# Kernel tuning notes

Hardware: AMD Instinct MI355X
Metric: run time of the kernel (lower is better)

Reference implementation:

```python
import jax, jax.numpy as jnp
import numpy as np

B, S, E, H = 8, 2048, 1024, 64

def setup_inputs() -> dict:
    key = jax.random.key(0)
    k1, k2, k3, k4 = jax.random.split(key, 4)
    scale = 0.02
    return {
        "x": jax.random.normal(k1, (B, S, E), dtype=jnp.float32),
        "Wq": jax.random.normal(k2, (E, H), dtype=jnp.float32) * scale,
        "Wk": jax.random.normal(k3, (E, H), dtype=jnp.float32) * scale,
        "Wv": jax.random.normal(k4, (E, H), dtype=jnp.float32) * scale,
    }

def reference(x, Wq, Wk, Wv):
    # x: [B, S, E]; projections to [B, S, H]
    q = jnp.einsum("bse,eh->bsh", x, Wq)
    k = jnp.einsum("bse,eh->bsh", x, Wk)
    v = jnp.einsum("bse,eh->bsh", x, Wv)
    head_size = Wq.shape[1]
    # NOTE: original divides by head_size (not sqrt(head_size))
    scores = jnp.einsum("bqh,bkh->bqk", q, k) / head_size  # [B, S, S]
    seq = q.shape[1]
    causal = jnp.tril(jnp.ones((seq, seq), dtype=bool))
    scores = jnp.where(causal, scores, -jnp.inf)
    attn = jax.nn.softmax(scores, axis=-1)
    # dropout p=0.0 (eval) -> identity
    return jnp.einsum("bqk,bkh->bqh", attn, v)
```

## Files before the change

### kernel.cpp

```cpp
#include <hip/hip_runtime.h>


typedef __bf16 bf16;
typedef bf16 bf16x8 __attribute__((ext_vector_type(8)));
typedef bf16 bf16x4 __attribute__((ext_vector_type(4)));
typedef float v4f __attribute__((ext_vector_type(4)));

#define MFMA_BF16 __builtin_amdgcn_mfma_f32_16x16x32_bf16

constexpr int SEQ = 2048, EDIM = 1024, HDIM = 64;
constexpr float SCALE_L2E = 1.4426950408889634f / 64.0f;

__global__ __launch_bounds__(256) void prep_w_kernel(
    const float* __restrict__ Wq, const float* __restrict__ Wk,
    const float* __restrict__ Wv, bf16* __restrict__ Wt) {
  int mat = blockIdx.x >> 5, kseg = blockIdx.x & 31;
  const float* src = mat == 0 ? Wq : (mat == 1 ? Wk : Wv);
  int n = threadIdx.x & 63;
  int k0 = kseg * 32 + (threadIdx.x >> 6) * 8;
  bf16x8 v;
#pragma unroll
  for (int j = 0; j < 8; ++j)
    v[j] = (bf16)src[(k0 + j) * 64 + n];
  *reinterpret_cast<bf16x8*>(Wt + (size_t)(mat * 64 + n) * EDIM + k0) = v;
}

__global__ __launch_bounds__(256) void proj_kernel(
    const float* __restrict__ x, const bf16* __restrict__ Wt,
    bf16* __restrict__ qw, bf16* __restrict__ kw, bf16* __restrict__ vT) {
  const int t = threadIdx.x;
  const int w = t >> 6, lane = t & 63, quad = lane >> 4, l16 = lane & 15;
  const int mi = w & 1, nh = w >> 1;
  const int m0 = blockIdx.x * 32;
  const int row = m0 + 16 * mi + l16;

  const float* xr = x + (size_t)row * EDIM + 8 * quad;
  const bf16* wB = Wt + (size_t)(96 * nh + l16) * EDIM + 8 * quad;

  v4f acc[6] = {};
  float4 aA[2][4];
  bf16x8 bReg[2][12];

  auto loadA = [&](int kk, int slot) {
    const float* p = xr + kk * 64;
    aA[slot][0] = *reinterpret_cast<const float4*>(p);
    aA[slot][1] = *reinterpret_cast<const float4*>(p + 4);
    aA[slot][2] = *reinterpret_cast<const float4*>(p + 32);
    aA[slot][3] = *reinterpret_cast<const float4*>(p + 36);
  };
  auto loadB = [&](int kk, int slot) {
#pragma unroll
    for (int nt = 0; nt < 6; ++nt)
#pragma unroll
      for (int ks = 0; ks < 2; ++ks)
        bReg[slot][2 * nt + ks] = *reinterpret_cast<const bf16x8*>(
            wB + (size_t)(16 * nt) * EDIM + kk * 64 + 32 * ks);
  };

  loadA(0, 0);
  loadB(0, 0);
  loadA(1, 1);
  loadB(1, 1);

#pragma unroll 2
  for (int kk = 0; kk < 16; ++kk) {
    const int buf = kk & 1;
    bf16x8 af[2];
#pragma unroll
    for (int ks = 0; ks < 2; ++ks) {
      float4 lo = aA[buf][2 * ks], hi = aA[buf][2 * ks + 1];
      af[ks][0] = (bf16)lo.x; af[ks][1] = (bf16)lo.y;
      af[ks][2] = (bf16)lo.z; af[ks][3] = (bf16)lo.w;
      af[ks][4] = (bf16)hi.x; af[ks][5] = (bf16)hi.y;
      af[ks][6] = (bf16)hi.z; af[ks][7] = (bf16)hi.w;
    }
    if (kk + 2 < 16) loadA(kk + 2, buf);
#pragma unroll
    for (int nt = 0; nt < 6; ++nt)
#pragma unroll
      for (int ks = 0; ks < 2; ++ks)
        acc[nt] = MFMA_BF16(af[ks], bReg[buf][2 * nt + ks], acc[nt], 0, 0, 0);
    if (kk + 2 < 16) loadB(kk + 2, buf);
  }

  const int token0 = m0 + 16 * mi + 4 * quad;
#pragma unroll
  for (int nt = 0; nt < 6; ++nt) {
    const int tl = 6 * nh + nt;
    if (tl < 4) {
      const int n = 16 * tl + l16;
#pragma unroll
      for (int r = 0; r < 4; ++r)
        qw[(size_t)(token0 + r) * HDIM + n] = (bf16)acc[nt][r];
    } else if (tl < 8) {
      const int n = 16 * (tl - 4) + l16;
#pragma unroll
      for (int r = 0; r < 4; ++r)
        kw[(size_t)(token0 + r) * HDIM + n] = (bf16)acc[nt][r];
    } else {
      const int hrow = 16 * (tl - 8) + l16;
      const int b = token0 >> 11, s0 = token0 & 2047;
      bf16x4 pk = {(bf16)acc[nt][0], (bf16)acc[nt][1], (bf16)acc[nt][2],
                   (bf16)acc[nt][3]};
      *reinterpret_cast<bf16x4*>(vT + ((size_t)(b * 64 + hrow)) * SEQ + s0) =
          pk;
    }
  }
}

__global__ __launch_bounds__(256) void attn_kernel(
    const bf16* __restrict__ qw, const bf16* __restrict__ kw,
    const bf16* __restrict__ vT, float* __restrict__ out) {
  const int batch = blockIdx.x & 7;
  const int pi = blockIdx.x >> 3;
  const int w = threadIdx.x >> 6;
  const int lane = threadIdx.x & 63;
  const int quad = lane >> 4, l16 = lane & 15;

  __shared__ __align__(16) bf16 p_lds[4][2][32][68];
  __shared__ __align__(16) float o_lds[3][32][68];
  __shared__ float l_lds[3][32];

  const bf16* qB = qw + (size_t)batch * SEQ * HDIM;
  const bf16* kB = kw + (size_t)batch * SEQ * HDIM;
  const bf16* vB = vT + (size_t)batch * HDIM * SEQ;

  for (int sp = 0; sp < 2; ++sp) {
    const int j = sp ? (63 - pi) : pi;
    const int q0 = 32 * j;
    const int T64 = (j + 2) >> 1;
    const int nw = (T64 > w) ? (((T64 - 1 - w) >> 2) + 1) : 0;

    bf16x8 aq[2][2];
#pragma unroll
    for (int mi = 0; mi < 2; ++mi)
#pragma unroll
      for (int kf = 0; kf < 2; ++kf)
        aq[mi][kf] = *reinterpret_cast<const bf16x8*>(
            qB + (size_t)(q0 + 16 * mi + l16) * HDIM + 32 * kf + 8 * quad);

    v4f accO[2][4] = {};
    float l_part[2][4] = {{0.f, 0.f, 0.f, 0.f}, {0.f, 0.f, 0.f, 0.f}};
    bf16x8 kfr[4][2];

    auto loadK = [&](int jt) {
#pragma unroll
      for (int nt = 0; nt < 4; ++nt)
#pragma unroll
        for (int kf = 0; kf < 2; ++kf)
          kfr[nt][kf] = *reinterpret_cast<const bf16x8*>(
              kB + (size_t)(64 * jt + 16 * nt + l16) * HDIM + 32 * kf +
              8 * quad);
    };
    auto qk_exp_stage = [&](int jt, int slot) {
      v4f s[2][4] = {};
#pragma unroll
      for (int mi = 0; mi < 2; ++mi)
#pragma unroll
        for (int nt = 0; nt < 4; ++nt) {
          s[mi][nt] = MFMA_BF16(aq[mi][0], kfr[nt][0], s[mi][nt], 0, 0, 0);
          s[mi][nt] = MFMA_BF16(aq[mi][1], kfr[nt][1], s[mi][nt], 0, 0, 0);
        }
      const bool last = (jt == T64 - 1);
#pragma unroll
      for (int mi = 0; mi < 2; ++mi)
#pragma unroll
        for (int nt = 0; nt < 4; ++nt)
#pragma unroll
          for (int r = 0; r < 4; ++r) {
            float p = __builtin_amdgcn_exp2f(s[mi][nt][r] * SCALE_L2E);
            if (last &&
                (64 * jt + 16 * nt + l16 > q0 + 16 * mi + 4 * quad + r))
              p = 0.f;
            l_part[mi][r] += p;
            p_lds[w][slot][16 * mi + 4 * quad + r][16 * nt + l16] = (bf16)p;
          }
    };

    if (nw > 0) {
      loadK(w);
      qk_exp_stage(w, 0);
    }
    for (int i = 0; i < nw; ++i) {
      const int jt = w + 4 * i;
      const int k0 = 64 * jt;
      if (i + 1 < nw) loadK(jt + 4);
      bf16x8 vfr[4][2];
#pragma unroll
      for (int nt = 0; nt < 4; ++nt)
#pragma unroll
        for (int kc = 0; kc < 2; ++kc)
          vfr[nt][kc] = *reinterpret_cast<const bf16x8*>(
              vB + (size_t)(16 * nt + l16) * SEQ + k0 + 32 * kc + 8 * quad);
      asm volatile("s_waitcnt lgkmcnt(0)" ::: "memory");
      bf16x8 pa[2][2];
#pragma unroll
      for (int mi = 0; mi < 2; ++mi)
#pragma unroll
        for (int kc = 0; kc < 2; ++kc)
          pa[mi][kc] = *reinterpret_cast<const bf16x8*>(
              &p_lds[w][i & 1][16 * mi + l16][32 * kc + 8 * quad]);
      if (i + 1 < nw) qk_exp_stage(jt + 4, (i + 1) & 1);
#pragma unroll
      for (int mi = 0; mi < 2; ++mi)
#pragma unroll
        for (int nt = 0; nt < 4; ++nt) {
          accO[mi][nt] = MFMA_BF16(pa[mi][0], vfr[nt][0], accO[mi][nt], 0, 0, 0);
          accO[mi][nt] = MFMA_BF16(pa[mi][1], vfr[nt][1], accO[mi][nt], 0, 0, 0);
        }
    }

#pragma unroll
    for (int mi = 0; mi < 2; ++mi)
#pragma unroll
      for (int r = 0; r < 4; ++r) {
        float s = l_part[mi][r];
        s += __shfl_xor(s, 1, 16);
        s += __shfl_xor(s, 2, 16);
        s += __shfl_xor(s, 4, 16);
        s += __shfl_xor(s, 8, 16);
        l_part[mi][r] = s;
      }

    __syncthreads();
    if (w > 0) {
#pragma unroll
      for (int mi = 0; mi < 2; ++mi)
#pragma unroll
        for (int nt = 0; nt < 4; ++nt)
#pragma unroll
          for (int r = 0; r < 4; ++r)
            o_lds[w - 1][16 * mi + 4 * quad + r][16 * nt + l16] =
                accO[mi][nt][r];
      if (l16 == 0) {
#pragma unroll
        for (int mi = 0; mi < 2; ++mi)
#pragma unroll
          for (int r = 0; r < 4; ++r)
            l_lds[w - 1][16 * mi + 4 * quad + r] = l_part[mi][r];
      }
    }
    __syncthreads();
    if (w == 0) {
#pragma unroll
      for (int mi = 0; mi < 2; ++mi)
#pragma unroll
        for (int r = 0; r < 4; ++r) {
          const int row = 16 * mi + 4 * quad + r;
          float lt = l_part[mi][r] + l_lds[0][row] + l_lds[1][row] +
                     l_lds[2][row];
          float inv = 1.0f / lt;
          float* op = out + ((size_t)batch * SEQ + q0 + row) * HDIM;
#pragma unroll
          for (int nt = 0; nt < 4; ++nt)
            op[16 * nt + l16] =
                (accO[mi][nt][r] + o_lds[0][row][16 * nt + l16] +
                 o_lds[1][row][16 * nt + l16] +
                 o_lds[2][row][16 * nt + l16]) *
                inv;
        }
    }
  }
}

extern "C" void kernel_launch(void* const* d_in, const int* in_sizes, int n_in,
                              void* d_out, int out_size, void* d_ws,
                              size_t ws_size, hipStream_t stream) {
  const float* x = (const float*)d_in[0];
  const float* Wq = (const float*)d_in[1];
  const float* Wk = (const float*)d_in[2];
  const float* Wv = (const float*)d_in[3];

  char* ws = (char*)d_ws;
  bf16* Wt = (bf16*)(ws);
  bf16* qw = (bf16*)(ws + 0x60000);
  bf16* kw = (bf16*)(ws + 0x260000);
  bf16* vT = (bf16*)(ws + 0x460000);

  prep_w_kernel<<<96, 256, 0, stream>>>(Wq, Wk, Wv, Wt);
  proj_kernel<<<512, 256, 0, stream>>>(x, Wt, qw, kw, vT);
  attn_kernel<<<256, 256, 0, stream>>>(qw, kw, vT, (float*)d_out);
}
```

Baseline: 168.0 us.

## Pre-swizzle weights, K and V into MFMA fragment order and stage x via LDS

Weights are written in MFMA-fragment order so each lane loads a contiguous 16-byte chunk. The projection kernel now loads x rows with coalesced float4 reads, converts them to bf16 and stages them in double-buffered LDS before the fragment reads. A new swizzle kernel rewrites K and V into fragment-contiguous layout so the attention loads coalesce. This adds an extra launch and an extra pass over K and V, and the LDS staging in the projection kernel has no explicit barrier between the write and the read.

```diff
diff --git a/kernel.cpp b/kernel.cpp
--- a/kernel.cpp
+++ b/kernel.cpp
@@ -13,40 +13,47 @@
 
 __global__ __launch_bounds__(256) void prep_w_kernel(
     const float* __restrict__ Wq, const float* __restrict__ Wk,
-    const float* __restrict__ Wv, bf16* __restrict__ Wt) {
-  int mat = blockIdx.x >> 5, kseg = blockIdx.x & 31;
-  const float* src = mat == 0 ? Wq : (mat == 1 ? Wk : Wv);
-  int n = threadIdx.x & 63;
-  int k0 = kseg * 32 + (threadIdx.x >> 6) * 8;
+    const float* __restrict__ Wv, bf16* __restrict__ WtF) {
+  const int tg = blockIdx.x * 256 + threadIdx.x;
+  const int lane = tg & 63, f = tg >> 6;
+  const int kk = f / 24, rem = f % 24, ntl = rem >> 1, ks = rem & 1;
+  const int q = lane >> 4, l16 = lane & 15;
+  const float* src = (ntl < 4) ? Wq : ((ntl < 8) ? Wk : Wv);
+  const int n = (ntl & 3) * 16 + l16;
+  const int k0 = kk * 64 + 32 * ks + 8 * q;
   bf16x8 v;
 #pragma unroll
-  for (int j = 0; j < 8; ++j)
-    v[j] = (bf16)src[(k0 + j) * 64 + n];
-  *reinterpret_cast<bf16x8*>(Wt + (size_t)(mat * 64 + n) * EDIM + k0) = v;
-}
-
-__global__ __launch_bounds__(256) void proj_kernel(
-    const float* __restrict__ x, const bf16* __restrict__ Wt,
+  for (int j = 0; j < 8; ++j) v[j] = (bf16)src[(k0 + j) * 64 + n];
+  *reinterpret_cast<bf16x8*>(WtF + (size_t)tg * 8) = v;
+}
+
+__global__ __launch_bounds__(256, 2) void proj_kernel(
+    const float* __restrict__ x, const bf16* __restrict__ WtF,
     bf16* __restrict__ qw, bf16* __restrict__ kw, bf16* __restrict__ vT) {
+  __shared__ __align__(16) bf16 As[2][4][16][72];
+
   const int t = threadIdx.x;
   const int w = t >> 6, lane = t & 63, quad = lane >> 4, l16 = lane & 15;
   const int mi = w & 1, nh = w >> 1;
   const int m0 = blockIdx.x * 32;
-  const int row = m0 + 16 * mi + l16;
-
-  const float* xr = x + (size_t)row * EDIM + 8 * quad;
-  const bf16* wB = Wt + (size_t)(96 * nh + l16) * EDIM + 8 * quad;
+
+  const int srow = lane >> 2, scol = (lane & 3) * 16;
+  const float* xs = x + (size_t)(m0 + 16 * mi + srow) * EDIM + scol;
 
   v4f acc[6] = {};
-  float4 aA[2][4];
+  float4 aReg[2][2];
   bf16x8 bReg[2][12];
 
   auto loadA = [&](int kk, int slot) {
-    const float* p = xr + kk * 64;
-    aA[slot][0] = *reinterpret_cast<const float4*>(p);
-    aA[slot][1] = *reinterpret_cast<const float4*>(p + 4);
-    aA[slot][2] = *reinterpret_cast<const float4*>(p + 32);
-    aA[slot][3] = *reinterpret_cast<const float4*>(p + 36);
+    const float* p = xs + kk * 64;
+    aReg[slot][0] = *reinterpret_cast<const float4*>(p);
+    aReg[slot][1] = *reinterpret_cast<const float4*>(p + 4);
+  };
+  float4 aReg2[2][2];
+  auto loadA2 = [&](int kk, int slot) {
+    const float* p = xs + kk * 64 + 8;
+    aReg2[slot][0] = *reinterpret_cast<const float4*>(p);
+    aReg2[slot][1] = *reinterpret_cast<const float4*>(p + 4);
   };
   auto loadB = [&](int kk, int slot) {
 #pragma unroll
@@ -54,33 +61,42 @@
 #pragma unroll
       for (int ks = 0; ks < 2; ++ks)
         bReg[slot][2 * nt + ks] = *reinterpret_cast<const bf16x8*>(
-            wB + (size_t)(16 * nt) * EDIM + kk * 64 + 32 * ks);
+            WtF +
+            (size_t)((kk * 24 + (6 * nh + nt) * 2 + ks) * 64 + lane) * 8);
   };
-
-  loadA(0, 0);
-  loadB(0, 0);
-  loadA(1, 1);
-  loadB(1, 1);
+  auto commitA = [&](int slot, int buf) {
+    bf16x8 h0, h1;
+#pragma unroll
+    for (int e = 0; e < 4; ++e) {
+      h0[e] = (bf16)(&aReg[slot][0].x)[e];
+      h0[4 + e] = (bf16)(&aReg[slot][1].x)[e];
+      h1[e] = (bf16)(&aReg2[slot][0].x)[e];
+      h1[4 + e] = (bf16)(&aReg2[slot][1].x)[e];
+    }
+    *reinterpret_cast<bf16x8*>(&As[buf][w][srow][scol]) = h0;
+    *reinterpret_cast<bf16x8*>(&As[buf][w][srow][scol + 8]) = h1;
+  };
+
+  loadA(0, 0); loadA2(0, 0); loadB(0, 0);
+  loadA(1, 1); loadA2(1, 1); loadB(1, 1);
+  commitA(0, 0);
 
 #pragma unroll 2
   for (int kk = 0; kk < 16; ++kk) {
     const int buf = kk & 1;
     bf16x8 af[2];
 #pragma unroll
-    for (int ks = 0; ks < 2; ++ks) {
-      float4 lo = aA[buf][2 * ks], hi = aA[buf][2 * ks + 1];
-      af[ks][0] = (bf16)lo.x; af[ks][1] = (bf16)lo.y;
-      af[ks][2] = (bf16)lo.z; af[ks][3] = (bf16)lo.w;
-      af[ks][4] = (bf16)hi.x; af[ks][5] = (bf16)hi.y;
-      af[ks][6] = (bf16)hi.z; af[ks][7] = (bf16)hi.w;
-    }
-    if (kk + 2 < 16) loadA(kk + 2, buf);
+    for (int ks = 0; ks < 2; ++ks)
+      af[ks] = *reinterpret_cast<const bf16x8*>(
+          &As[buf][w][l16][32 * ks + 8 * quad]);
+    if (kk + 2 < 16) { loadA(kk + 2, buf); loadA2(kk + 2, buf); }
 #pragma unroll
     for (int nt = 0; nt < 6; ++nt)
 #pragma unroll
       for (int ks = 0; ks < 2; ++ks)
         acc[nt] = MFMA_BF16(af[ks], bReg[buf][2 * nt + ks], acc[nt], 0, 0, 0);
     if (kk + 2 < 16) loadB(kk + 2, buf);
+    if (kk + 1 < 16) commitA(buf ^ 1, buf ^ 1);
   }
 
   const int token0 = m0 + 16 * mi + 4 * quad;
@@ -108,9 +124,37 @@
   }
 }
 
+__global__ __launch_bounds__(256) void swz_kernel(
+    const bf16* __restrict__ kw, const bf16* __restrict__ vT,
+    bf16* __restrict__ kswz, bf16* __restrict__ vswz) {
+  const int batch = blockIdx.x & 7;
+  const int jt = blockIdx.x >> 3;
+  const int t = threadIdx.x, lane = t & 63;
+  const int q = lane >> 4, l16 = lane & 15;
+  const bf16* kB = kw + (size_t)batch * SEQ * HDIM;
+  const bf16* vB = vT + (size_t)batch * HDIM * SEQ;
+  bf16* kS = kswz + (size_t)batch * 131072;
+  bf16* vS = vswz + (size_t)batch * 131072;
+#pragma unroll
+  for (int rep = 0; rep < 4; ++rep) {
+    const int fi = rep * 4 + (t >> 6);
+    const int nt = (fi & 7) >> 1, h = fi & 1;
+    bf16x8 v;
+    if (fi < 8)
+      v = *reinterpret_cast<const bf16x8*>(
+          kB + (size_t)(64 * jt + 16 * nt + l16) * HDIM + 32 * h + 8 * q);
+    else
+      v = *reinterpret_cast<const bf16x8*>(
+          vB + (size_t)(16 * nt + l16) * SEQ + 64 * jt + 32 * h + 8 * q);
+    bf16* dst = (fi < 8) ? kS : vS;
+    *reinterpret_cast<bf16x8*>(
+        dst + (size_t)((jt * 8 + nt * 2 + h) * 64 + lane) * 8) = v;
+  }
+}
+
 __global__ __launch_bounds__(256) void attn_kernel(
-    const bf16* __restrict__ qw, const bf16* __restrict__ kw,
-    const bf16* __restrict__ vT, float* __restrict__ out) {
+    const bf16* __restrict__ qw, const bf16* __restrict__ kswz,
+    const bf16* __restrict__ vswz, float* __restrict__ out) {
   const int batch = blockIdx.x & 7;
   const int pi = blockIdx.x >> 3;
   const int w = threadIdx.x >> 6;
@@ -122,8 +166,8 @@
   __shared__ float l_lds[3][32];
 
   const bf16* qB = qw + (size_t)batch * SEQ * HDIM;
-  const bf16* kB = kw + (size_t)batch * SEQ * HDIM;
-  const bf16* vB = vT + (size_t)batch * HDIM * SEQ;
+  const bf16* kS = kswz + (size_t)batch * 131072;
+  const bf16* vS = vswz + (size_t)batch * 131072;
 
   for (int sp = 0; sp < 2; ++sp) {
     const int j = sp ? (63 - pi) : pi;
@@ -149,8 +193,7 @@
 #pragma unroll
         for (int kf = 0; kf < 2; ++kf)
           kfr[nt][kf] = *reinterpret_cast<const bf16x8*>(
-              kB + (size_t)(64 * jt + 16 * nt + l16) * HDIM + 32 * kf +
-              8 * quad);
+              kS + (size_t)((jt * 8 + nt * 2 + kf) * 64 + lane) * 8);
     };
     auto qk_exp_stage = [&](int jt, int slot) {
       v4f s[2][4] = {};
@@ -183,7 +226,6 @@
     }
     for (int i = 0; i < nw; ++i) {
       const int jt = w + 4 * i;
-      const int k0 = 64 * jt;
       if (i + 1 < nw) loadK(jt + 4);
       bf16x8 vfr[4][2];
 #pragma unroll
@@ -191,7 +233,7 @@
 #pragma unroll
         for (int kc = 0; kc < 2; ++kc)
           vfr[nt][kc] = *reinterpret_cast<const bf16x8*>(
-              vB + (size_t)(16 * nt + l16) * SEQ + k0 + 32 * kc + 8 * quad);
+              vS + (size_t)((jt * 8 + nt * 2 + kc) * 64 + lane) * 8);
       asm volatile("s_waitcnt lgkmcnt(0)" ::: "memory");
       bf16x8 pa[2][2];
 #pragma unroll
@@ -272,12 +314,15 @@
   const float* Wv = (const float*)d_in[3];
 
   char* ws = (char*)d_ws;
-  bf16* Wt = (bf16*)(ws);
+  bf16* WtF = (bf16*)(ws);
   bf16* qw = (bf16*)(ws + 0x60000);
   bf16* kw = (bf16*)(ws + 0x260000);
   bf16* vT = (bf16*)(ws + 0x460000);
-
-  prep_w_kernel<<<96, 256, 0, stream>>>(Wq, Wk, Wv, Wt);
-  proj_kernel<<<512, 256, 0, stream>>>(x, Wt, qw, kw, vT);
-  attn_kernel<<<256, 256, 0, stream>>>(qw, kw, vT, (float*)d_out);
-}
+  bf16* kswz = (bf16*)(ws + 0x660000);
+  bf16* vswz = (bf16*)(ws + 0x860000);
+
+  prep_w_kernel<<<96, 256, 0, stream>>>(Wq, Wk, Wv, WtF);
+  proj_kernel<<<512, 256, 0, stream>>>(x, WtF, qw, kw, vT);
+  swz_kernel<<<256, 256, 0, stream>>>(kw, vT, kswz, vswz);
+  attn_kernel<<<256, 256, 0, stream>>>(qw, kswz, vswz, (float*)d_out);
+}
```

New measurement: 144.5 us. -14.0%, faster.
